# Optimization experiments

Measured on AMD Instinct MI355X. Metric: run time of the kernel, lower is better.

## Reference

```python
import jax, jax.numpy as jnp
import numpy as np

B, N_N, N_E, C, H = 1, 50000, 250000, 128, 128
NNZ = 2 * N_E


def _layernorm(x, g, b, eps=1e-5):
    mu = jnp.mean(x, axis=-1, keepdims=True)
    var = jnp.mean((x - mu) ** 2, axis=-1, keepdims=True)
    return (x - mu) * jax.lax.rsqrt(var + eps) * g + b


def setup_inputs() -> dict:
    key = jax.random.key(0)
    ks = jax.random.split(key, 12)
    f32 = jnp.float32
    inp = {
        "node": jax.random.normal(ks[0], (B, N_N, C), f32),
        "edge": jax.random.normal(ks[1], (B, N_E, C), f32),
        "edgeIdx": jax.random.randint(ks[2], (N_E, 2), 0, N_N),
        "e2n_rows": jax.random.randint(ks[3], (NNZ,), 0, N_N),
        "e2n_cols": jax.random.randint(ks[4], (NNZ,), 0, N_E),
        "e2n_vals": jnp.ones((NNZ,), f32),
        # norm1 over 3C, norm2 over 2C
        "norm1_g": jnp.ones((3 * C,), f32),
        "norm1_b": jnp.zeros((3 * C,), f32),
        "norm2_g": jnp.ones((2 * C,), f32),
        "norm2_b": jnp.zeros((2 * C,), f32),
        # mlpEdge: 3C -> 3H -> C ; mlpNode: 2C -> 2H -> C (weights stored [in,out])
        "e_w1": jax.random.normal(ks[5], (3 * C, 3 * H), f32) / np.sqrt(3 * C).astype(np.float32),
        "e_b1": jnp.zeros((3 * H,), f32),
        "e_w2": jax.random.normal(ks[6], (3 * H, C), f32) / np.sqrt(3 * H).astype(np.float32),
        "e_b2": jnp.zeros((C,), f32),
        "n_w1": jax.random.normal(ks[7], (2 * C, 2 * H), f32) / np.sqrt(2 * C).astype(np.float32),
        "n_b1": jnp.zeros((2 * H,), f32),
        "n_w2": jax.random.normal(ks[8], (2 * H, C), f32) / np.sqrt(2 * H).astype(np.float32),
        "n_b2": jnp.zeros((C,), f32),
    }
    return inp


def reference(node, edge, edgeIdx, e2n_rows, e2n_cols, e2n_vals,
              norm1_g, norm1_b, norm2_g, norm2_b,
              e_w1, e_b1, e_w2, e_b2, n_w1, n_b1, n_w2, n_b2):
    Bv, Nn, Cc = node.shape
    Ne = edge.shape[1]
    # gather both endpoints of each edge: [B, N_e, 2, C] -> [B, N_e, 2C]
    gathered = node[:, edgeIdx].reshape(Bv, Ne, 2 * Cc)
    e = jnp.concatenate([edge, gathered], axis=-1)           # [B, N_e, 3C]
    e = _layernorm(e, norm1_g, norm1_b)
    e = jax.nn.gelu(e @ e_w1 + e_b1, approximate=False) @ e_w2 + e_b2  # [B, N_e, C]
    e_h = e.astype(jnp.float16)                              # matches .half() in torch
    # sparse matmul edge2node @ edge  == scatter-add over COO nnz
    msg = e_h.transpose(1, 0, 2)[e2n_cols] * e2n_vals.astype(jnp.float16)[:, None, None]  # [nnz, B, C]
    agg = jax.ops.segment_sum(msg, e2n_rows, num_segments=Nn)  # [N_n, B, C]
    node_agg = agg.transpose(1, 0, 2).astype(node.dtype)       # [B, N_n, C]
    n = jnp.concatenate([node, node_agg], axis=-1)             # [B, N_n, 2C]
    n = _layernorm(n, norm2_g, norm2_b)
    n = jax.nn.gelu(n @ n_w1 + n_b1, approximate=False) @ n_w2 + n_b2
    node_out = node + n
    edge_out = edge + e_h.astype(edge.dtype)
    return node_out, edge_out
```

## Files before the change

### kernel.cpp

```cpp
#include <hip/hip_runtime.h>
#include <hip/hip_fp16.h>

typedef unsigned short u16;
typedef unsigned int u32;

#define N_NODE 50000
#define N_EDGE 250000
#define NNZV   500000
#define RCAP   48
#define OVFCAP 4096

typedef __attribute__((ext_vector_type(8))) __bf16 bf16x8;
typedef __attribute__((ext_vector_type(4))) float f32x4;

#define WAITLGKM0() asm volatile("s_waitcnt lgkmcnt(0)" ::: "memory")
#define SBAR() __builtin_amdgcn_s_barrier()
#define SCHEDB() __builtin_amdgcn_sched_barrier(0)

static __device__ __forceinline__ u16 f2bf(float f) {
  union { float f; u32 u; } cv; cv.f = f;
  u32 u = cv.u;
  return (u16)((u + 0x7FFFu + ((u >> 16) & 1u)) >> 16);
}

static __device__ __forceinline__ u32 pk_bf16(float lo, float hi) {
  u32 r;
  asm("v_cvt_pk_bf16_f32 %0, %1, %2" : "=v"(r) : "v"(lo), "v"(hi));
  return r;
}

static __device__ __forceinline__ u16 f2bf_fast(float x) {
  return (u16)pk_bf16(x, x);
}

template<typename T>
static __device__ __forceinline__ T ldo(const void* base, u32 off) {
  return *(const T*)((const char*)base + off);
}
template<typename T>
static __device__ __forceinline__ void sto(void* base, u32 off, T v) {
  *(T*)((char*)base + off) = v;
}

static __device__ __forceinline__ float gelu_f(float x) {
  float z = fabsf(x) * 0.70710678118654752f;
  float t = __builtin_amdgcn_rcpf(1.0f + 0.3275911f * z);
  float p = t * (0.254829592f + t * (-0.284496736f + t * (1.421413741f +
            t * (-1.453152027f + t * 1.061405429f))));
  float er = 1.0f - p * __expf(-z * z);
  er = copysignf(er, x);
  return 0.5f * x * (1.0f + er);
}

static __device__ __forceinline__ void wconv(const float* __restrict__ in,
                                             u16* __restrict__ out,
                                             int K, int N, int cpw, int idx) {
  int k = idx / N, n = idx % N;
  int w = n / cpw, rem = n % cpw;
  int t = rem >> 4, l15 = rem & 15;
  int ks = k >> 5, gq = (k >> 3) & 3, e = k & 7;
  int steps = K >> 5, tiles = cpw >> 4;
  size_t o = ((((size_t)(w * steps + ks) * tiles + t) * 64) + gq * 16 + l15) * 8 + e;
  out[o] = f2bf(in[(size_t)k * N + n]);
}

__global__ __launch_bounds__(256) void prep_kernel(
    const float* __restrict__ ew1, const float* __restrict__ ew2,
    const float* __restrict__ nw1, const float* __restrict__ nw2,
    u16* __restrict__ ew1r, u16* __restrict__ ew2r,
    u16* __restrict__ nw1r, u16* __restrict__ nw2r,
    u32* __restrict__ rcnt0) {
  const int S1 = 384 * 384, S2 = 384 * 128, S3 = 256 * 256, S4 = 256 * 128;
  const int SC = N_NODE + 1;
  const long total = (long)S1 + S2 + S3 + S4 + SC;
  for (long i = (long)blockIdx.x * 256 + threadIdx.x; i < total;
       i += (long)gridDim.x * 256) {
    long idx = i;
    if (idx < S1) { wconv(ew1, ew1r, 384, 384, 48, (int)idx); continue; }
    idx -= S1;
    if (idx < S2) { wconv(ew2, ew2r, 384, 128, 16, (int)idx); continue; }
    idx -= S2;
    if (idx < S3) { wconv(nw1, nw1r, 256, 256, 32, (int)idx); continue; }
    idx -= S3;
    if (idx < S4) { wconv(nw2, nw2r, 256, 128, 16, (int)idx); continue; }
    idx -= S4;
    rcnt0[idx] = 0;
  }
}

__global__ __launch_bounds__(256) void fill_row_kernel(
    const int* __restrict__ rows, const int* __restrict__ cols,
    const float* __restrict__ vals,
    u32* __restrict__ rcnt, int2* __restrict__ buck, int4* __restrict__ ovf) {
  int k = blockIdx.x * 256 + threadIdx.x;
  if (k >= NNZV) return;
  int r = rows[k];
  u32 p = atomicAdd(&rcnt[r], 1u);
  if (p < RCAP) {
    buck[(size_t)r * RCAP + p] = make_int2(cols[k], __float_as_int(vals[k]));
  } else {
    u32 q = atomicAdd(&rcnt[N_NODE], 1u);
    if (q < OVFCAP) ovf[q] = make_int4(r, cols[k], __float_as_int(vals[k]), 0);
  }
}

__global__ __launch_bounds__(256) void agg_gather_kernel(
    const u32* __restrict__ rcnt, const int2* __restrict__ buck,
    const __half* __restrict__ e_h, __half* __restrict__ agg) {
  int r = __builtin_amdgcn_readfirstlane(blockIdx.x * 4 + (threadIdx.x >> 6));
  if (r >= N_NODE) return;
  int l = threadIdx.x & 63;
  u32 n = rcnt[r]; if (n > RCAP) n = RCAP;
  const int2* bp = buck + (size_t)r * RCAP;
  float a0 = 0.0f, a1 = 0.0f;
  for (u32 p = 0; p < n; p += 4) {
    int2 e0 = bp[p];
    int2 e1 = bp[p + 1];
    int2 e2 = bp[p + 2];
    int2 e3 = bp[p + 3];
    if (p + 1 >= n) e1 = make_int2(e0.x, 0);
    if (p + 2 >= n) e2 = make_int2(e0.x, 0);
    if (p + 3 >= n) e3 = make_int2(e0.x, 0);
    __half2 h0 = ldo<__half2>(e_h, (u32)e0.x * 256 + l * 4);
    __half2 h1 = ldo<__half2>(e_h, (u32)e1.x * 256 + l * 4);
    __half2 h2 = ldo<__half2>(e_h, (u32)e2.x * 256 + l * 4);
    __half2 h3 = ldo<__half2>(e_h, (u32)e3.x * 256 + l * 4);
    float2 f0 = __half22float2(h0), f1 = __half22float2(h1);
    float2 f2 = __half22float2(h2), f3 = __half22float2(h3);
    float v0 = __int_as_float(e0.y), v1 = __int_as_float(e1.y);
    float v2 = __int_as_float(e2.y), v3 = __int_as_float(e3.y);
    a0 = fmaf(f0.x, v0, a0); a1 = fmaf(f0.y, v0, a1);
    a0 = fmaf(f1.x, v1, a0); a1 = fmaf(f1.y, v1, a1);
    a0 = fmaf(f2.x, v2, a0); a1 = fmaf(f2.y, v2, a1);
    a0 = fmaf(f3.x, v3, a0); a1 = fmaf(f3.y, v3, a1);
  }
  *(__half2*)&agg[(size_t)r * 128 + 2 * l] = __floats2half2_rn(a0, a1);
}

__global__ __launch_bounds__(256) void ovf_scatter_kernel(
    const int4* __restrict__ ovf, const u32* __restrict__ rcnt,
    const __half* __restrict__ e_h, __half* __restrict__ agg) {
  int n = (int)rcnt[N_NODE]; if (n > OVFCAP) n = OVFCAP;
  int wv = blockIdx.x * 4 + (threadIdx.x >> 6);
  int l = threadIdx.x & 63;
  for (int q = wv; q < n; q += gridDim.x * 4) {
    int4 e = ovf[q];
    __half2 hv = *(const __half2*)&e_h[(size_t)e.y * 128 + 2 * l];
    __half2 h2 = __hmul2(hv, __float2half2_rn(__int_as_float(e.z)));
    unsafeAtomicAdd((__half2*)&agg[(size_t)e.x * 128 + 2 * l], h2);
  }
}

__global__ __launch_bounds__(512, 4) void edge_fused_kernel(
    const float* __restrict__ node, const float* __restrict__ edge,
    const int* __restrict__ edgeIdx,
    const float* __restrict__ lng, const float* __restrict__ lnb,
    const u16* __restrict__ w1r, const float* __restrict__ b1,
    const u16* __restrict__ w2r, const float* __restrict__ b2,
    __half* __restrict__ e_h, float* __restrict__ out_edge) {
  const int lane = threadIdx.x & 63, wid = threadIdx.x >> 6;
  const int l15 = lane & 15, gq = lane >> 4;
  const int row0 = blockIdx.x * 64;

  __shared__ __align__(16) u16 xp[64 * 384];
  __shared__ __align__(16) float er[64 * 128];

  const bf16x8* w1v = (const bf16x8*)w1r + (size_t)wid * (12 * 192) + lane;
  bf16x8 br[3][3];
#define LDB1(s, b) { br[b][0] = w1v[(s) * 192]; br[b][1] = w1v[(s) * 192 + 64]; \
                     br[b][2] = w1v[(s) * 192 + 128]; }
  LDB1(0, 0); LDB1(1, 1); LDB1(2, 2);

  float ga[6], be[6];
#pragma unroll
  for (int s = 0; s < 3; ++s) {
    float2 g2 = *(const float2*)&lng[s * 128 + 2 * lane];
    float2 b2v = *(const float2*)&lnb[s * 128 + 2 * lane];
    ga[2 * s] = g2.x; ga[2 * s + 1] = g2.y;
    be[2 * s] = b2v.x; be[2 * s + 1] = b2v.y;
  }
  {
    u32 oe[8], oa[8], ob[8];
#pragma unroll
    for (int t = 0; t < 8; ++t) {
      int g = row0 + wid * 8 + t; if (g > N_EDGE - 1) g = N_EDGE - 1;
      int2 ab = ldo<int2>(edgeIdx, (u32)g * 8);
      oe[t] = (u32)g * 512 + lane * 8;
      oa[t] = (u32)ab.x * 512 + lane * 8;
      ob[t] = (u32)ab.y * 512 + lane * 8;
    }
    float2 v0[8], v1[8], v2[8];
#pragma unroll
    for (int t = 0; t < 8; ++t) {
      v0[t] = ldo<float2>(edge, oe[t]);
      v1[t] = ldo<float2>(node, oa[t]);
      v2[t] = ldo<float2>(node, ob[t]);
    }
#pragma unroll
    for (int t = 0; t < 8; ++t) {
      int lr = wid * 8 + t;
      *(float2*)&er[lr * 128 + 2 * lane] = v0[t];
      float s  = v0[t].x + v0[t].y + v1[t].x + v1[t].y + v2[t].x + v2[t].y;
      float ss = v0[t].x*v0[t].x + v0[t].y*v0[t].y + v1[t].x*v1[t].x +
                 v1[t].y*v1[t].y + v2[t].x*v2[t].x + v2[t].y*v2[t].y;
#pragma unroll
      for (int m = 1; m < 64; m <<= 1) { s += __shfl_xor(s, m); ss += __shfl_xor(ss, m); }
      float mean = s * (1.0f / 384.0f);
      float var  = ss * (1.0f / 384.0f) - mean * mean;
      float rstd = rsqrtf(var + 1e-5f);
      float2 vv[3] = {v0[t], v1[t], v2[t]};
#pragma unroll
      for (int sg = 0; sg < 3; ++sg) {
        float y0 = (vv[sg].x - mean) * rstd * ga[2 * sg]     + be[2 * sg];
        float y1 = (vv[sg].y - mean) * rstd * ga[2 * sg + 1] + be[2 * sg + 1];
        int sl = (sg * 16 + (lane >> 2)) ^ (lr & 15);
        *(u32*)&xp[lr * 384 + sl * 8 + (lane & 3) * 2] = pk_bf16(y0, y1);
      }
    }
  }
  WAITLGKM0(); SCHEDB(); SBAR(); SCHEDB();

  f32x4 acc1[4][3];
#pragma unroll
  for (int nt = 0; nt < 3; ++nt) {
    float bv = b1[wid * 48 + nt * 16 + l15];
#pragma unroll
    for (int m = 0; m < 4; ++m) acc1[m][nt] = (f32x4){bv, bv, bv, bv};
  }
  int aoff[4];
#pragma unroll
  for (int m = 0; m < 4; ++m) aoff[m] = (m * 16 + l15) * 384;

#pragma unroll
  for (int s = 0; s < 12; ++s) {
    const int axi = ((s * 4 + gq) ^ l15) * 8;
    bf16x8 a[4];
#pragma unroll
    for (int m = 0; m < 4; ++m) a[m] = *(const bf16x8*)&xp[aoff[m] + axi];
    __builtin_amdgcn_s_setprio(1);
#pragma unroll
    for (int m = 0; m < 4; ++m)
#pragma unroll
      for (int nt = 0; nt < 3; ++nt)
        acc1[m][nt] = __builtin_amdgcn_mfma_f32_16x16x32_bf16(a[m], br[s % 3][nt], acc1[m][nt], 0, 0, 0);
    __builtin_amdgcn_s_setprio(0);
    if (s + 3 < 12) { LDB1(s + 3, s % 3); }
  }
  SCHEDB(); SBAR(); SCHEDB();

  const bf16x8* w2v = (const bf16x8*)w2r + (size_t)wid * (12 * 64) + lane;
  bf16x8 br2[3];
#define LDB2(s, b) { br2[b] = w2v[(s) * 64]; }
  LDB2(0, 0); LDB2(1, 1); LDB2(2, 2);
#pragma unroll
  for (int m = 0; m < 4; ++m)
#pragma unroll
    for (int nt = 0; nt < 3; ++nt) {
      const int c = wid * 48 + nt * 16 + l15;
#pragma unroll
      for (int j = 0; j < 4; ++j) {
        int r = m * 16 + gq * 4 + j;
        xp[r * 384 + (((c >> 3) ^ (r & 15)) * 8) + (c & 7)] = f2bf_fast(gelu_f(acc1[m][nt][j]));
      }
    }
  WAITLGKM0(); SCHEDB(); SBAR(); SCHEDB();

  float b2v = b2[wid * 16 + l15];
  f32x4 acc2[4];
#pragma unroll
  for (int m = 0; m < 4; ++m) acc2[m] = (f32x4){b2v, b2v, b2v, b2v};

#pragma unroll
  for (int g = 0; g < 12; ++g) {
    const int axi = ((g * 4 + gq) ^ l15) * 8;
    bf16x8 a[4];
#pragma unroll
    for (int m = 0; m < 4; ++m) a[m] = *(const bf16x8*)&xp[aoff[m] + axi];
    __builtin_amdgcn_s_setprio(1);
#pragma unroll
    for (int m = 0; m < 4; ++m)
      acc2[m] = __builtin_amdgcn_mfma_f32_16x16x32_bf16(a[m], br2[g % 3], acc2[m], 0, 0, 0);
    __builtin_amdgcn_s_setprio(0);
    if (g + 3 < 12) { LDB2(g + 3, g % 3); }
  }

  const int col = wid * 16 + l15;
#pragma unroll
  for (int m = 0; m < 4; ++m)
#pragma unroll
    for (int j = 0; j < 4; ++j) {
      int lr = m * 16 + gq * 4 + j;
      int r = row0 + lr;
      if (r < N_EDGE) {
        __half hv = __float2half(acc2[m][j]);
        sto<__half>(e_h, (u32)r * 256 + col * 2, hv);
        sto<float>(out_edge, (u32)r * 512 + col * 4, er[lr * 128 + col] + __half2float(hv));
      }
    }
#undef LDB1
#undef LDB2
}

__global__ __launch_bounds__(512, 4) void node_fused_kernel(
    const float* __restrict__ node, const __half* __restrict__ agg,
    const float* __restrict__ lng, const float* __restrict__ lnb,
    const u16* __restrict__ w1r, const float* __restrict__ b1,
    const u16* __restrict__ w2r, const float* __restrict__ b2,
    float* __restrict__ out_node) {
  const int lane = threadIdx.x & 63, wid = threadIdx.x >> 6;
  const int l15 = lane & 15, gq = lane >> 4;
  const int row0 = blockIdx.x * 64;

  __shared__ __align__(16) u16 xp[64 * 256];
  __shared__ __align__(16) float nr[64 * 128];

  const bf16x8* w1v = (const bf16x8*)w1r + (size_t)wid * (8 * 128) + lane;
  bf16x8 br[3][2];
#define NLDB1(s, b) { br[b][0] = w1v[(s) * 128]; br[b][1] = w1v[(s) * 128 + 64]; }
  NLDB1(0, 0); NLDB1(1, 1); NLDB1(2, 2);

  float ga[4], be[4];
#pragma unroll
  for (int s = 0; s < 2; ++s) {
    float2 g2 = *(const float2*)&lng[s * 128 + 2 * lane];
    float2 b2v = *(const float2*)&lnb[s * 128 + 2 * lane];
    ga[2 * s] = g2.x; ga[2 * s + 1] = g2.y;
    be[2 * s] = b2v.x; be[2 * s + 1] = b2v.y;
  }
  {
    float2 v0[8], v1[8];
#pragma unroll
    for (int t = 0; t < 8; ++t) {
      int g = row0 + wid * 8 + t; if (g > N_NODE - 1) g = N_NODE - 1;
      v0[t] = ldo<float2>(node, (u32)g * 512 + lane * 8);
      v1[t] = __half22float2(ldo<__half2>(agg, (u32)g * 256 + lane * 4));
    }
#pragma unroll
    for (int t = 0; t < 8; ++t) {
      int lr = wid * 8 + t;
      *(float2*)&nr[lr * 128 + 2 * lane] = v0[t];
      float s  = v0[t].x + v0[t].y + v1[t].x + v1[t].y;
      float ss = v0[t].x*v0[t].x + v0[t].y*v0[t].y + v1[t].x*v1[t].x + v1[t].y*v1[t].y;
#pragma unroll
      for (int m = 1; m < 64; m <<= 1) { s += __shfl_xor(s, m); ss += __shfl_xor(ss, m); }
      float mean = s * (1.0f / 256.0f);
      float var  = ss * (1.0f / 256.0f) - mean * mean;
      float rstd = rsqrtf(var + 1e-5f);
      float2 vv[2] = {v0[t], v1[t]};
#pragma unroll
      for (int sg = 0; sg < 2; ++sg) {
        float y0 = (vv[sg].x - mean) * rstd * ga[2 * sg]     + be[2 * sg];
        float y1 = (vv[sg].y - mean) * rstd * ga[2 * sg + 1] + be[2 * sg + 1];
        int sl = (sg * 16 + (lane >> 2)) ^ (lr & 15);
        *(u32*)&xp[lr * 256 + sl * 8 + (lane & 3) * 2] = pk_bf16(y0, y1);
      }
    }
  }
  WAITLGKM0(); SCHEDB(); SBAR(); SCHEDB();

  f32x4 acc1[4][2];
#pragma unroll
  for (int nt = 0; nt < 2; ++nt) {
    float bv = b1[wid * 32 + nt * 16 + l15];
#pragma unroll
    for (int m = 0; m < 4; ++m) acc1[m][nt] = (f32x4){bv, bv, bv, bv};
  }
  int aoff[4];
#pragma unroll
  for (int m = 0; m < 4; ++m) aoff[m] = (m * 16 + l15) * 256;

#pragma unroll
  for (int s = 0; s < 8; ++s) {
    const int axi = ((s * 4 + gq) ^ l15) * 8;
    bf16x8 a[4];
#pragma unroll
    for (int m = 0; m < 4; ++m) a[m] = *(const bf16x8*)&xp[aoff[m] + axi];
    __builtin_amdgcn_s_setprio(1);
#pragma unroll
    for (int m = 0; m < 4; ++m)
#pragma unroll
      for (int nt = 0; nt < 2; ++nt)
        acc1[m][nt] = __builtin_amdgcn_mfma_f32_16x16x32_bf16(a[m], br[s % 3][nt], acc1[m][nt], 0, 0, 0);
    __builtin_amdgcn_s_setprio(0);
    if (s + 3 < 8) { NLDB1(s + 3, s % 3); }
  }
  SCHEDB(); SBAR(); SCHEDB();

  const bf16x8* w2v = (const bf16x8*)w2r + (size_t)wid * (8 * 64) + lane;
  bf16x8 br2[3];
#define NLDB2(s, b) { br2[b] = w2v[(s) * 64]; }
  NLDB2(0, 0); NLDB2(1, 1); NLDB2(2, 2);
#pragma unroll
  for (int m = 0; m < 4; ++m)
#pragma unroll
    for (int nt = 0; nt < 2; ++nt) {
      const int c = wid * 32 + nt * 16 + l15;
#pragma unroll
      for (int j = 0; j < 4; ++j) {
        int r = m * 16 + gq * 4 + j;
        xp[r * 256 + (((c >> 3) ^ (r & 15)) * 8) + (c & 7)] = f2bf_fast(gelu_f(acc1[m][nt][j]));
      }
    }
  WAITLGKM0(); SCHEDB(); SBAR(); SCHEDB();

  float b2v = b2[wid * 16 + l15];
  f32x4 acc2[4];
#pragma unroll
  for (int m = 0; m < 4; ++m) acc2[m] = (f32x4){b2v, b2v, b2v, b2v};

#pragma unroll
  for (int g = 0; g < 8; ++g) {
    const int axi = ((g * 4 + gq) ^ l15) * 8;
    bf16x8 a[4];
#pragma unroll
    for (int m = 0; m < 4; ++m) a[m] = *(const bf16x8*)&xp[aoff[m] + axi];
    __builtin_amdgcn_s_setprio(1);
#pragma unroll
    for (int m = 0; m < 4; ++m)
      acc2[m] = __builtin_amdgcn_mfma_f32_16x16x32_bf16(a[m], br2[g % 3], acc2[m], 0, 0, 0);
    __builtin_amdgcn_s_setprio(0);
    if (g + 3 < 8) { NLDB2(g + 3, g % 3); }
  }

  const int col = wid * 16 + l15;
#pragma unroll
  for (int m = 0; m < 4; ++m)
#pragma unroll
    for (int j = 0; j < 4; ++j) {
      int lr = m * 16 + gq * 4 + j;
      int r = row0 + lr;
      if (r < N_NODE) {
        sto<float>(out_node, (u32)r * 512 + col * 4, nr[lr * 128 + col] + acc2[m][j]);
      }
    }
#undef NLDB1
#undef NLDB2
}

extern "C" void kernel_launch(void* const* d_in, const int* in_sizes, int n_in,
                              void* d_out, int out_size, void* d_ws, size_t ws_size,
                              hipStream_t stream) {
  (void)in_sizes; (void)n_in; (void)out_size; (void)ws_size;
  const float* node    = (const float*)d_in[0];
  const float* edge    = (const float*)d_in[1];
  const int*   edgeIdx = (const int*)d_in[2];
  const int*   e2n_r   = (const int*)d_in[3];
  const int*   e2n_c   = (const int*)d_in[4];
  const float* e2n_v   = (const float*)d_in[5];
  const float* n1g     = (const float*)d_in[6];
  const float* n1b     = (const float*)d_in[7];
  const float* n2g     = (const float*)d_in[8];
  const float* n2b     = (const float*)d_in[9];
  const float* ew1     = (const float*)d_in[10];
  const float* eb1     = (const float*)d_in[11];
  const float* ew2     = (const float*)d_in[12];
  const float* eb2     = (const float*)d_in[13];
  const float* nw1     = (const float*)d_in[14];
  const float* nb1     = (const float*)d_in[15];
  const float* nw2     = (const float*)d_in[16];
  const float* nb2     = (const float*)d_in[17];

  float* out_node = (float*)d_out;
  float* out_edge = out_node + (size_t)N_NODE * 128;

  char* w = (char*)d_ws;
  auto alloc = [&](size_t bytes) { char* p = w; w += (bytes + 255) & ~(size_t)255; return p; };
  u16* ew1r = (u16*)alloc((size_t)384 * 384 * 2);
  u16* ew2r = (u16*)alloc((size_t)384 * 128 * 2);
  u16* nw1r = (u16*)alloc((size_t)256 * 256 * 2);
  u16* nw2r = (u16*)alloc((size_t)256 * 128 * 2);
  __half* agg = (__half*)alloc((size_t)N_NODE * 128 * 2);
  __half* e_h = (__half*)alloc((size_t)N_EDGE * 128 * 2);
  u32* rcnt = (u32*)alloc((size_t)(N_NODE + 1) * 4);
  int4* ovf = (int4*)alloc((size_t)OVFCAP * 16);
  int2* buck = (int2*)alloc(((size_t)N_NODE * RCAP + 64) * 8);

  prep_kernel<<<1024, 256, 0, stream>>>(ew1, ew2, nw1, nw2,
                                        ew1r, ew2r, nw1r, nw2r, rcnt);

  fill_row_kernel<<<(NNZV + 255) / 256, 256, 0, stream>>>(
      e2n_r, e2n_c, e2n_v, rcnt, buck, ovf);

  edge_fused_kernel<<<(N_EDGE + 63) / 64, 512, 0, stream>>>(
      node, edge, edgeIdx, n1g, n1b, ew1r, eb1, ew2r, eb2, e_h, out_edge);

  agg_gather_kernel<<<(N_NODE + 3) / 4, 256, 0, stream>>>(rcnt, buck, e_h, agg);

  ovf_scatter_kernel<<<16, 256, 0, stream>>>(ovf, rcnt, e_h, agg);

  node_fused_kernel<<<(N_NODE + 63) / 64, 512, 0, stream>>>(
      node, agg, n2g, n2b, nw1r, nb1, nw2r, nb2, out_node);
}
```

Measured before the change: 291.9 us.

## Fuse sparse aggregation gather into node MLP kernel, drop agg buffer

```diff
diff --git a/kernel.cpp b/kernel.cpp
--- a/kernel.cpp
+++ b/kernel.cpp
@@ -104,53 +104,6 @@
   }
 }
 
-__global__ __launch_bounds__(256) void agg_gather_kernel(
-    const u32* __restrict__ rcnt, const int2* __restrict__ buck,
-    const __half* __restrict__ e_h, __half* __restrict__ agg) {
-  int r = __builtin_amdgcn_readfirstlane(blockIdx.x * 4 + (threadIdx.x >> 6));
-  if (r >= N_NODE) return;
-  int l = threadIdx.x & 63;
-  u32 n = rcnt[r]; if (n > RCAP) n = RCAP;
-  const int2* bp = buck + (size_t)r * RCAP;
-  float a0 = 0.0f, a1 = 0.0f;
-  for (u32 p = 0; p < n; p += 4) {
-    int2 e0 = bp[p];
-    int2 e1 = bp[p + 1];
-    int2 e2 = bp[p + 2];
-    int2 e3 = bp[p + 3];
-    if (p + 1 >= n) e1 = make_int2(e0.x, 0);
-    if (p + 2 >= n) e2 = make_int2(e0.x, 0);
-    if (p + 3 >= n) e3 = make_int2(e0.x, 0);
-    __half2 h0 = ldo<__half2>(e_h, (u32)e0.x * 256 + l * 4);
-    __half2 h1 = ldo<__half2>(e_h, (u32)e1.x * 256 + l * 4);
-    __half2 h2 = ldo<__half2>(e_h, (u32)e2.x * 256 + l * 4);
-    __half2 h3 = ldo<__half2>(e_h, (u32)e3.x * 256 + l * 4);
-    float2 f0 = __half22float2(h0), f1 = __half22float2(h1);
-    float2 f2 = __half22float2(h2), f3 = __half22float2(h3);
-    float v0 = __int_as_float(e0.y), v1 = __int_as_float(e1.y);
-    float v2 = __int_as_float(e2.y), v3 = __int_as_float(e3.y);
-    a0 = fmaf(f0.x, v0, a0); a1 = fmaf(f0.y, v0, a1);
-    a0 = fmaf(f1.x, v1, a0); a1 = fmaf(f1.y, v1, a1);
-    a0 = fmaf(f2.x, v2, a0); a1 = fmaf(f2.y, v2, a1);
-    a0 = fmaf(f3.x, v3, a0); a1 = fmaf(f3.y, v3, a1);
-  }
-  *(__half2*)&agg[(size_t)r * 128 + 2 * l] = __floats2half2_rn(a0, a1);
-}
-
-__global__ __launch_bounds__(256) void ovf_scatter_kernel(
-    const int4* __restrict__ ovf, const u32* __restrict__ rcnt,
-    const __half* __restrict__ e_h, __half* __restrict__ agg) {
-  int n = (int)rcnt[N_NODE]; if (n > OVFCAP) n = OVFCAP;
-  int wv = blockIdx.x * 4 + (threadIdx.x >> 6);
-  int l = threadIdx.x & 63;
-  for (int q = wv; q < n; q += gridDim.x * 4) {
-    int4 e = ovf[q];
-    __half2 hv = *(const __half2*)&e_h[(size_t)e.y * 128 + 2 * l];
-    __half2 h2 = __hmul2(hv, __float2half2_rn(__int_as_float(e.z)));
-    unsafeAtomicAdd((__half2*)&agg[(size_t)e.x * 128 + 2 * l], h2);
-  }
-}
-
 __global__ __launch_bounds__(512, 4) void edge_fused_kernel(
     const float* __restrict__ node, const float* __restrict__ edge,
     const int* __restrict__ edgeIdx,
@@ -302,7 +255,9 @@
 }
 
 __global__ __launch_bounds__(512, 4) void node_fused_kernel(
-    const float* __restrict__ node, const __half* __restrict__ agg,
+    const float* __restrict__ node, const __half* __restrict__ e_h,
+    const u32* __restrict__ rcnt, const int2* __restrict__ buck,
+    const int4* __restrict__ ovf,
     const float* __restrict__ lng, const float* __restrict__ lnb,
     const u16* __restrict__ w1r, const float* __restrict__ b1,
     const u16* __restrict__ w2r, const float* __restrict__ b2,
@@ -333,10 +288,57 @@
     for (int t = 0; t < 8; ++t) {
       int g = row0 + wid * 8 + t; if (g > N_NODE - 1) g = N_NODE - 1;
       v0[t] = ldo<float2>(node, (u32)g * 512 + lane * 8);
-      v1[t] = __half22float2(ldo<__half2>(agg, (u32)g * 256 + lane * 4));
-    }
-#pragma unroll
-    for (int t = 0; t < 8; ++t) {
+    }
+#pragma unroll 2
+    for (int t = 0; t < 8; ++t) {
+      int g = row0 + wid * 8 + t; if (g > N_NODE - 1) g = N_NODE - 1;
+      u32 n = rcnt[g]; if (n > RCAP) n = RCAP;
+      const int2* bp = buck + (size_t)g * RCAP;
+      float a0 = 0.0f, a1 = 0.0f;
+      for (u32 p = 0; p < n; p += 4) {
+        int2 e0 = bp[p];
+        int2 e1 = bp[p + 1];
+        int2 e2 = bp[p + 2];
+        int2 e3 = bp[p + 3];
+        if (p + 1 >= n) e1 = make_int2(e0.x, 0);
+        if (p + 2 >= n) e2 = make_int2(e0.x, 0);
+        if (p + 3 >= n) e3 = make_int2(e0.x, 0);
+        __half2 h0 = ldo<__half2>(e_h, (u32)e0.x * 256 + lane * 4);
+        __half2 h1 = ldo<__half2>(e_h, (u32)e1.x * 256 + lane * 4);
+        __half2 h2 = ldo<__half2>(e_h, (u32)e2.x * 256 + lane * 4);
+        __half2 h3 = ldo<__half2>(e_h, (u32)e3.x * 256 + lane * 4);
+        float2 f0 = __half22float2(h0), f1 = __half22float2(h1);
+        float2 f2 = __half22float2(h2), f3 = __half22float2(h3);
+        float w0 = __int_as_float(e0.y), w1_ = __int_as_float(e1.y);
+        float w2_ = __int_as_float(e2.y), w3 = __int_as_float(e3.y);
+        a0 = fmaf(f0.x, w0, a0); a1 = fmaf(f0.y, w0, a1);
+        a0 = fmaf(f1.x, w1_, a0); a1 = fmaf(f1.y, w1_, a1);
+        a0 = fmaf(f2.x, w2_, a0); a1 = fmaf(f2.y, w2_, a1);
+        a0 = fmaf(f3.x, w3, a0); a1 = fmaf(f3.y, w3, a1);
+      }
+      v1[t] = make_float2(a0, a1);
+    }
+    {
+      u32 novf = rcnt[N_NODE];
+      if (novf) {
+        if (novf > OVFCAP) novf = OVFCAP;
+        for (u32 q = 0; q < novf; ++q) {
+          int4 e = ovf[q];
+          int t = e.x - (row0 + wid * 8);
+          if (t >= 0 && t < 8) {
+            __half2 hv = ldo<__half2>(e_h, (u32)e.y * 256 + lane * 4);
+            float v = __int_as_float(e.z);
+            float2 f = __half22float2(hv);
+#pragma unroll
+            for (int tt = 0; tt < 8; ++tt)
+              if (tt == t) { v1[tt].x += f.x * v; v1[tt].y += f.y * v; }
+          }
+        }
+      }
+    }
+#pragma unroll
+    for (int t = 0; t < 8; ++t) {
+      v1[t] = __half22float2(__floats2half2_rn(v1[t].x, v1[t].y));
       int lr = wid * 8 + t;
       *(float2*)&nr[lr * 128 + 2 * lane] = v0[t];
       float s  = v0[t].x + v0[t].y + v1[t].x + v1[t].y;
@@ -469,7 +471,6 @@
   u16* ew2r = (u16*)alloc((size_t)384 * 128 * 2);
   u16* nw1r = (u16*)alloc((size_t)256 * 256 * 2);
   u16* nw2r = (u16*)alloc((size_t)256 * 128 * 2);
-  __half* agg = (__half*)alloc((size_t)N_NODE * 128 * 2);
   __half* e_h = (__half*)alloc((size_t)N_EDGE * 128 * 2);
   u32* rcnt = (u32*)alloc((size_t)(N_NODE + 1) * 4);
   int4* ovf = (int4*)alloc((size_t)OVFCAP * 16);
@@ -484,10 +485,6 @@
   edge_fused_kernel<<<(N_EDGE + 63) / 64, 512, 0, stream>>>(
       node, edge, edgeIdx, n1g, n1b, ew1r, eb1, ew2r, eb2, e_h, out_edge);
 
-  agg_gather_kernel<<<(N_NODE + 3) / 4, 256, 0, stream>>>(rcnt, buck, e_h, agg);
-
-  ovf_scatter_kernel<<<16, 256, 0, stream>>>(ovf, rcnt, e_h, agg);
-
   node_fused_kernel<<<(N_NODE + 63) / 64, 512, 0, stream>>>(
-      node, agg, n2g, n2b, nw1r, nb1, nw2r, nb2, out_node);
-}
+      node, e_h, rcnt, buck, ovf, n2g, n2b, nw1r, nb1, nw2r, nb2, out_node);
+}
```

Result: slower. 312.9 us (+7.2%).
